# Performance work log

Hardware: AMD Instinct MI355X
Metric: run time of the kernel (lower is better)

Reference implementation:

```python
import jax, jax.numpy as jnp
import numpy as np

LAMADA = 0.0001
USER_NUM, ITEM_NUM, FACTOR = 100000, 50000, 64
N_EDGES, BATCH = 3200000, 4096


def setup_inputs() -> dict:
    key = jax.random.key(0)
    ks = jax.random.split(key, 11)
    return {
        "embed_user": jax.random.normal(ks[0], (USER_NUM, FACTOR), jnp.float32) * 0.01,
        "embed_item": jax.random.normal(ks[1], (ITEM_NUM, FACTOR), jnp.float32) * 0.01,
        "u_idx": jax.random.randint(ks[2], (N_EDGES,), 0, USER_NUM, jnp.int32),
        "i_idx": jax.random.randint(ks[3], (N_EDGES,), 0, ITEM_NUM, jnp.int32),
        "ui_vals": jax.random.uniform(ks[4], (N_EDGES,), jnp.float32),
        "iu_vals": jax.random.uniform(ks[5], (N_EDGES,), jnp.float32),
        "d_i": jax.random.uniform(ks[6], (USER_NUM,), jnp.float32),
        "d_j": jax.random.uniform(ks[7], (ITEM_NUM,), jnp.float32),
        "user": jax.random.randint(ks[8], (BATCH,), 0, USER_NUM, jnp.int32),
        "item_i": jax.random.randint(ks[9], (BATCH,), 0, ITEM_NUM, jnp.int32),
        "item_j": jax.random.randint(ks[10], (BATCH,), 0, ITEM_NUM, jnp.int32),
    }


def _spmm_u(i_emb, u_idx, i_idx, vals):
    # user_item_matrix @ items_embedding  (COO SpMM via segment_sum)
    msg = i_emb[i_idx] * vals[:, None]  # [E, F]
    return jax.ops.segment_sum(msg, u_idx, num_segments=USER_NUM)


def _spmm_i(u_emb, u_idx, i_idx, vals):
    # item_user_matrix @ users_embedding
    msg = u_emb[u_idx] * vals[:, None]  # [E, F]
    return jax.ops.segment_sum(msg, i_idx, num_segments=ITEM_NUM)


def reference(embed_user, embed_item, u_idx, i_idx, ui_vals, iu_vals,
              d_i, d_j, user, item_i, item_j):
    di = d_i[:, None]  # [U,1] broadcast == expand(-1, factor_num)
    dj = d_j[:, None]  # [I,1]

    gcn1_u = _spmm_u(embed_item, u_idx, i_idx, ui_vals) + embed_user * di
    gcn1_i = _spmm_i(embed_user, u_idx, i_idx, iu_vals) + embed_item * dj
    gcn2_u = _spmm_u(gcn1_i, u_idx, i_idx, ui_vals) + gcn1_u * di
    gcn2_i = _spmm_i(gcn1_u, u_idx, i_idx, iu_vals) + gcn1_i * dj

    gcn_u = embed_user + gcn1_u + gcn2_u
    gcn_i = embed_item + gcn1_i + gcn2_i

    u = gcn_u[user]        # [B, F]
    pi = gcn_i[item_i]     # [B, F]
    pj = gcn_i[item_j]     # [B, F]

    pred_i = jnp.sum(u * pi, axis=-1)
    pred_j = jnp.sum(u * pj, axis=-1)

    l2 = LAMADA * jnp.mean(u ** 2) + LAMADA * jnp.mean(pi ** 2 + pj ** 2)
    # -log(sigmoid(x)) == softplus(-x), numerically stable
    loss2 = jnp.mean(jax.nn.softplus(-(pred_i - pred_j)))
    return loss2 + l2
```

## Files before the change

### kernel.cpp

```cpp
#include <hip/hip_runtime.h>
#include <math.h>

#define USER_NUM 100000
#define ITEM_NUM 50000
#define FACTOR   64
#define LAMADA   0.0001f

#define RB_BITS 7
#define RB      128
#define NBU   782
#define NBI   391
#define CAPU  5120
#define CAPI  9216
#define CHUNK 8192

#define FP8_SCALE    256.0f
#define FP8_INVSCALE 0.00390625f

typedef unsigned short ushort_t;
typedef unsigned int   uint_t;
typedef float v2f_t __attribute__((ext_vector_type(2)));

__device__ __forceinline__ void dec8(uint2 t, float* __restrict__ f) {
    v2f_t p0 = __builtin_amdgcn_cvt_pk_f32_fp8(t.x, false);
    v2f_t p1 = __builtin_amdgcn_cvt_pk_f32_fp8(t.x, true);
    v2f_t p2 = __builtin_amdgcn_cvt_pk_f32_fp8(t.y, false);
    v2f_t p3 = __builtin_amdgcn_cvt_pk_f32_fp8(t.y, true);
    f[0] = p0.x; f[1] = p0.y; f[2] = p1.x; f[3] = p1.y;
    f[4] = p2.x; f[5] = p2.y; f[6] = p3.x; f[7] = p3.y;
}
__device__ __forceinline__ uint_t enc1(float v) {
    return (uint_t)__builtin_amdgcn_cvt_pk_fp8_f32(v, v, 0, false) & 0xFFu;
}
__device__ __forceinline__ float decv(uint_t e) {
    v2f_t p = __builtin_amdgcn_cvt_pk_f32_fp8(e, false);
    return p.x;
}

__device__ __forceinline__ void acc8p(uint2 t, float v, v2f_t* __restrict__ S) {
    v2f_t vv = {v, v};
    S[0] = __builtin_elementwise_fma(vv, __builtin_amdgcn_cvt_pk_f32_fp8(t.x, false), S[0]);
    S[1] = __builtin_elementwise_fma(vv, __builtin_amdgcn_cvt_pk_f32_fp8(t.x, true),  S[1]);
    S[2] = __builtin_elementwise_fma(vv, __builtin_amdgcn_cvt_pk_f32_fp8(t.y, false), S[2]);
    S[3] = __builtin_elementwise_fma(vv, __builtin_amdgcn_cvt_pk_f32_fp8(t.y, true),  S[3]);
}

__global__ void to_fp8_both(const float* __restrict__ a, int n4a,
                            const float* __restrict__ b, int n4b,
                            unsigned char* __restrict__ da, unsigned char* __restrict__ db) {
    int gid = blockIdx.x * blockDim.x + threadIdx.x;
    const float* src; unsigned char* dst; int idx;
    if (gid < n4a) { src = a; dst = da; idx = gid; }
    else if (gid < n4a + n4b) { src = b; dst = db; idx = gid - n4a; }
    else return;
    float4 v = ((const float4*)src)[idx];
    int r = __builtin_amdgcn_cvt_pk_fp8_f32(v.x * FP8_SCALE, v.y * FP8_SCALE, 0, false);
    r = __builtin_amdgcn_cvt_pk_fp8_f32(v.z * FP8_SCALE, v.w * FP8_SCALE, r, true);
    ((uint_t*)dst)[idx] = (uint_t)r;
}

__global__ void init_cursors(int* __restrict__ cur_u, int* __restrict__ cur_i) {
    int t = blockIdx.x * blockDim.x + threadIdx.x;
    if (t < NBU) cur_u[t] = t * CAPU;
    if (t < NBI) cur_i[t] = t * CAPI;
}

__device__ __forceinline__ void place_phase(
    const int* __restrict__ rows_idx, const int* __restrict__ cols_idx,
    const float* __restrict__ vals, int* __restrict__ cur,
    uint_t* __restrict__ staged, int nb, int start, int end,
    uint_t* __restrict__ s_stage, int* __restrict__ s_cnt,
    int* __restrict__ s_scan, int* __restrict__ s_gbase) {
    int tid = threadIdx.x;
    int len = end - start;
    s_cnt[tid] = 0;
    __syncthreads();
    int vend = start + (len & ~3);
    for (int e = start + tid * 4; e < vend; e += 4096) {
        int4 r = *(const int4*)(rows_idx + e);
        atomicAdd(&s_cnt[r.x >> RB_BITS], 1);
        atomicAdd(&s_cnt[r.y >> RB_BITS], 1);
        atomicAdd(&s_cnt[r.z >> RB_BITS], 1);
        atomicAdd(&s_cnt[r.w >> RB_BITS], 1);
    }
    for (int e = vend + tid; e < end; e += 1024) {
        atomicAdd(&s_cnt[rows_idx[e] >> RB_BITS], 1);
    }
    __syncthreads();
    int c = s_cnt[tid];
    s_scan[tid] = c;
    __syncthreads();
    #pragma unroll
    for (int off = 1; off < 1024; off <<= 1) {
        int v = (tid >= off) ? s_scan[tid - off] : 0;
        __syncthreads();
        s_scan[tid] += v;
        __syncthreads();
    }
    int excl = s_scan[tid] - c;
    __syncthreads();
    s_scan[tid] = excl;
    if (tid < nb) {
        s_gbase[tid] = c ? atomicAdd(&cur[tid], c) : 0;
        s_cnt[tid] = excl;
    }
    __syncthreads();
    for (int e = start + tid * 4; e < vend; e += 4096) {
        int4 r = *(const int4*)(rows_idx + e);
        int4 cc = *(const int4*)(cols_idx + e);
        float4 v = *(const float4*)(vals + e);
        int p0 = atomicAdd(&s_cnt[r.x >> RB_BITS], 1);
        int p1 = atomicAdd(&s_cnt[r.y >> RB_BITS], 1);
        int p2 = atomicAdd(&s_cnt[r.z >> RB_BITS], 1);
        int p3 = atomicAdd(&s_cnt[r.w >> RB_BITS], 1);
        s_stage[p0] = ((uint_t)(r.x & (RB-1)) << 25) | ((uint_t)cc.x << 8) | enc1(v.x);
        s_stage[p1] = ((uint_t)(r.y & (RB-1)) << 25) | ((uint_t)cc.y << 8) | enc1(v.y);
        s_stage[p2] = ((uint_t)(r.z & (RB-1)) << 25) | ((uint_t)cc.z << 8) | enc1(v.z);
        s_stage[p3] = ((uint_t)(r.w & (RB-1)) << 25) | ((uint_t)cc.w << 8) | enc1(v.w);
    }
    for (int e = vend + tid; e < end; e += 1024) {
        int rr = rows_idx[e];
        int p = atomicAdd(&s_cnt[rr >> RB_BITS], 1);
        s_stage[p] = ((uint_t)(rr & (RB-1)) << 25) | ((uint_t)cols_idx[e] << 8) | enc1(vals[e]);
    }
    __syncthreads();
    for (int t = tid; t < len; t += 1024) {
        int lo = 0, hi = nb;
        while (hi - lo > 1) {
            int mid = (lo + hi) >> 1;
            if (s_scan[mid] <= t) lo = mid; else hi = mid;
        }
        staged[s_gbase[lo] + (t - s_scan[lo])] = s_stage[t];
    }
    __syncthreads();
}

__global__ __launch_bounds__(1024) void place2(
        const int* __restrict__ u_idx, const int* __restrict__ i_idx,
        const float* __restrict__ ui_vals, const float* __restrict__ iu_vals,
        int* __restrict__ cur_u, int* __restrict__ cur_i,
        uint_t* __restrict__ staged_u, uint_t* __restrict__ staged_i, int n_edges) {
    __shared__ uint_t s_stage[CHUNK];
    __shared__ int s_cnt[1024];
    __shared__ int s_scan[1025];
    __shared__ int s_gbase[1024];
    int start = blockIdx.x * CHUNK;
    int end = min(start + CHUNK, n_edges);
    if (start >= end) return;
    place_phase(u_idx, i_idx, ui_vals, cur_u, staged_u, NBU, start, end,
                s_stage, s_cnt, s_scan, s_gbase);
    place_phase(i_idx, u_idx, iu_vals, cur_i, staged_i, NBI, start, end,
                s_stage, s_cnt, s_scan, s_gbase);
}

__global__ void bucket_finalize(const uint_t* __restrict__ staged, const int* __restrict__ cur,
                                int cap, int* __restrict__ ptr, uint_t* __restrict__ cs,
                                int n_rows) {
    __shared__ int s_cnt[RB];
    __shared__ int s_pos[RB];
    int b = blockIdx.x, tid = threadIdx.x;
    int sbase = b * cap;
    int nE = cur[b] - sbase;
    if (tid < RB) s_cnt[tid] = 0;
    __syncthreads();
    int nE8 = nE & ~7;
    for (int k = tid * 8; k < nE8; k += 2048) {
        uint4 a = *(const uint4*)(staged + sbase + k);
        uint4 c = *(const uint4*)(staged + sbase + k + 4);
        atomicAdd(&s_cnt[a.x >> 25], 1); atomicAdd(&s_cnt[a.y >> 25], 1);
        atomicAdd(&s_cnt[a.z >> 25], 1); atomicAdd(&s_cnt[a.w >> 25], 1);
        atomicAdd(&s_cnt[c.x >> 25], 1); atomicAdd(&s_cnt[c.y >> 25], 1);
        atomicAdd(&s_cnt[c.z >> 25], 1); atomicAdd(&s_cnt[c.w >> 25], 1);
    }
    if (tid == 0) for (int k = nE8; k < nE; ++k) atomicAdd(&s_cnt[staged[sbase + k] >> 25], 1);
    __syncthreads();
    int x = (tid < RB) ? s_cnt[tid] : 0;
    if (tid < RB) s_pos[tid] = x;
    __syncthreads();
    for (int off = 1; off < RB; off <<= 1) {
        int t = (tid < RB && tid >= off) ? s_pos[tid - off] : 0;
        __syncthreads();
        if (tid < RB) s_pos[tid] += t;
        __syncthreads();
    }
    if (tid < RB) {
        int excl = s_pos[tid] - x + sbase;
        int r = (b << RB_BITS) + tid;
        if (r < n_rows) ptr[r + b] = excl;
        s_pos[tid] = excl;
    }
    if (tid == 0) ptr[min((b << RB_BITS) + RB, n_rows) + b] = sbase + nE;
    __syncthreads();
    for (int k = tid * 8; k < nE8; k += 2048) {
        uint4 a = *(const uint4*)(staged + sbase + k);
        uint4 c = *(const uint4*)(staged + sbase + k + 4);
        int p0 = atomicAdd(&s_pos[a.x >> 25], 1);
        int p1 = atomicAdd(&s_pos[a.y >> 25], 1);
        int p2 = atomicAdd(&s_pos[a.z >> 25], 1);
        int p3 = atomicAdd(&s_pos[a.w >> 25], 1);
        int p4 = atomicAdd(&s_pos[c.x >> 25], 1);
        int p5 = atomicAdd(&s_pos[c.y >> 25], 1);
        int p6 = atomicAdd(&s_pos[c.z >> 25], 1);
        int p7 = atomicAdd(&s_pos[c.w >> 25], 1);
        cs[p0] = a.x & 0x01FFFFFFu; cs[p1] = a.y & 0x01FFFFFFu;
        cs[p2] = a.z & 0x01FFFFFFu; cs[p3] = a.w & 0x01FFFFFFu;
        cs[p4] = c.x & 0x01FFFFFFu; cs[p5] = c.y & 0x01FFFFFFu;
        cs[p6] = c.z & 0x01FFFFFFu; cs[p7] = c.w & 0x01FFFFFFu;
    }
    if (tid == 0) for (int k = nE8; k < nE; ++k) {
        uint_t se = staged[sbase + k];
        int pos = atomicAdd(&s_pos[se >> 25], 1);
        cs[pos] = se & 0x01FFFFFFu;
    }
}

__device__ __forceinline__ void gather_dot8f8(const uint_t* __restrict__ cs, int start, int end,
                                              const uint2* __restrict__ tab2, int g, int l,
                                              float* __restrict__ acc) {
    v2f_t A[4] = {{0.f,0.f},{0.f,0.f},{0.f,0.f},{0.f,0.f}};
    v2f_t B[4] = {{0.f,0.f},{0.f,0.f},{0.f,0.f},{0.f,0.f}};
    const uint2* __restrict__ tl = tab2 + l;
    int k = start;
    for (; k + 32 <= end; k += 32) {
        uint_t c0 = cs[k + g];
        uint_t c1 = cs[k + 8 + g];
        uint_t c2 = cs[k + 16 + g];
        uint_t c3 = cs[k + 24 + g];
        uint2 t0 = tl[(c0 >> 8) << 3];
        uint2 t1 = tl[(c1 >> 8) << 3];
        uint2 t2 = tl[(c2 >> 8) << 3];
        uint2 t3 = tl[(c3 >> 8) << 3];
        float v0 = decv(c0);
        float v1 = decv(c1);
        float v2 = decv(c2);
        float v3 = decv(c3);
        acc8p(t0, v0, A);
        acc8p(t1, v1, B);
        acc8p(t2, v2, A);
        acc8p(t3, v3, B);
    }
    if (k + 16 <= end) {
        uint_t c0 = cs[k + g];
        uint_t c1 = cs[k + 8 + g];
        uint2 t0 = tl[(c0 >> 8) << 3];
        uint2 t1 = tl[(c1 >> 8) << 3];
        acc8p(t0, decv(c0), A);
        acc8p(t1, decv(c1), B);
        k += 16;
    }
    if (k + 8 <= end) {
        uint_t c0 = cs[k + g];
        uint2 t0 = tl[(c0 >> 8) << 3];
        acc8p(t0, decv(c0), A);
        k += 8;
    }
    if (k + g < end) {
        uint_t c0 = cs[k + g];
        uint2 t0 = tl[(c0 >> 8) << 3];
        acc8p(t0, decv(c0), B);
    }
    #pragma unroll
    for (int i = 0; i < 4; ++i) {
        v2f_t s = A[i] + B[i];
        float r0 = s.x, r1 = s.y;
        r0 += __shfl_xor(r0, 8, 64);
        r1 += __shfl_xor(r1, 8, 64);
        r0 += __shfl_xor(r0, 16, 64);
        r1 += __shfl_xor(r1, 16, 64);
        r0 += __shfl_xor(r0, 32, 64);
        r1 += __shfl_xor(r1, 32, 64);
        acc[2 * i]     = r0;
        acc[2 * i + 1] = r1;
    }
}

__global__ void csr_spmm5(const int* __restrict__ ptr_u, const uint_t* __restrict__ cs_u,
                          const int* __restrict__ ptr_i, const uint_t* __restrict__ cs_i,
                          const uint2* __restrict__ beu2, const uint2* __restrict__ bei2,
                          const float* __restrict__ eu, const float* __restrict__ ei,
                          const float* __restrict__ d_i, const float* __restrict__ d_j,
                          uint2* __restrict__ g1u2, uint2* __restrict__ g1i2) {
    int w = (blockIdx.x * blockDim.x + threadIdx.x) >> 6;
    int lane = threadIdx.x & 63;
    int g = lane >> 3, l = lane & 7;
    const int* ptr; const uint_t* cs; const uint2* src; const float* self;
    const float* d; uint2* out; int row;
    if (w < USER_NUM) {
        row = w; ptr = ptr_u; cs = cs_u; src = bei2; self = eu; d = d_i; out = g1u2;
    } else if (w < USER_NUM + ITEM_NUM) {
        row = w - USER_NUM; ptr = ptr_i; cs = cs_i; src = beu2; self = ei; d = d_j; out = g1i2;
    } else return;
    int pidx = row + (row >> RB_BITS);
    int start = ptr[pidx], end = ptr[pidx + 1];
    float acc[8];
    gather_dot8f8(cs, start, end, src, g, l, acc);
    if (g == 0) {
        float4 s0 = ((const float4*)self)[(size_t)row * 16 + l * 2];
        float4 s1 = ((const float4*)self)[(size_t)row * 16 + l * 2 + 1];
        float dv = d[row] * FP8_SCALE;
        float o0 = acc[0] + s0.x * dv, o1 = acc[1] + s0.y * dv;
        float o2 = acc[2] + s0.z * dv, o3 = acc[3] + s0.w * dv;
        float o4 = acc[4] + s1.x * dv, o5 = acc[5] + s1.y * dv;
        float o6 = acc[6] + s1.z * dv, o7 = acc[7] + s1.w * dv;
        int r0 = __builtin_amdgcn_cvt_pk_fp8_f32(o0, o1, 0, false);
        r0 = __builtin_amdgcn_cvt_pk_fp8_f32(o2, o3, r0, true);
        int r1 = __builtin_amdgcn_cvt_pk_fp8_f32(o4, o5, 0, false);
        r1 = __builtin_amdgcn_cvt_pk_fp8_f32(o6, o7, r1, true);
        uint2 o; o.x = (uint_t)r0; o.y = (uint_t)r1;
        out[(size_t)row * 8 + l] = o;
    }
}

__global__ void gather_rows(const float* __restrict__ eu, const float* __restrict__ ei,
                            const uint2* __restrict__ g1u2, const uint2* __restrict__ g1i2,
                            const int* __restrict__ ptr_u, const uint_t* __restrict__ cs_u,
                            const int* __restrict__ ptr_i, const uint_t* __restrict__ cs_i,
                            const float* __restrict__ d_i, const float* __restrict__ d_j,
                            const int* __restrict__ user, const int* __restrict__ item_i,
                            const int* __restrict__ item_j, float* __restrict__ rows, int batch) {
    int w = (blockIdx.x * blockDim.x + threadIdx.x) >> 6;
    int lane = threadIdx.x & 63;
    int g = lane >> 3, l = lane & 7;
    if (w >= 3 * batch) return;
    int role = w / batch;
    int s = w - role * batch;
    int row; const int* ptr; const uint_t* cs; const uint2* tab; const uint2* g1t;
    const float* self; float sc;
    if (role == 0) {
        row = user[s]; ptr = ptr_u; cs = cs_u; tab = g1i2; g1t = g1u2;
        self = eu; sc = 1.f + d_i[row];
    } else {
        row = (role == 1) ? item_i[s] : item_j[s];
        ptr = ptr_i; cs = cs_i; tab = g1u2; g1t = g1i2;
        self = ei; sc = 1.f + d_j[row];
    }
    int pidx = row + (row >> RB_BITS);
    float acc[8];
    gather_dot8f8(cs, ptr[pidx], ptr[pidx + 1], tab, g, l, acc);
    if (g == 0) {
        uint2 gg = g1t[(size_t)row * 8 + l];
        float gf[8];
        dec8(gg, gf);
        float4 e0 = ((const float4*)self)[(size_t)row * 16 + l * 2];
        float4 e1 = ((const float4*)self)[(size_t)row * 16 + l * 2 + 1];
        float4 o0, o1;
        o0.x = e0.x + (gf[0] * sc + acc[0]) * FP8_INVSCALE;
        o0.y = e0.y + (gf[1] * sc + acc[1]) * FP8_INVSCALE;
        o0.z = e0.z + (gf[2] * sc + acc[2]) * FP8_INVSCALE;
        o0.w = e0.w + (gf[3] * sc + acc[3]) * FP8_INVSCALE;
        o1.x = e1.x + (gf[4] * sc + acc[4]) * FP8_INVSCALE;
        o1.y = e1.y + (gf[5] * sc + acc[5]) * FP8_INVSCALE;
        o1.z = e1.z + (gf[6] * sc + acc[6]) * FP8_INVSCALE;
        o1.w = e1.w + (gf[7] * sc + acc[7]) * FP8_INVSCALE;
        ((float4*)rows)[(size_t)w * 16 + l * 2]     = o0;
        ((float4*)rows)[(size_t)w * 16 + l * 2 + 1] = o1;
    }
}

__global__ void loss_dots(const float* __restrict__ rows, float* __restrict__ partials,
                          int batch, int nblocks) {
    __shared__ float s_su2[4], s_sp2[4], s_sp[4];
    int w = (blockIdx.x * blockDim.x + threadIdx.x) >> 6;
    int lane = threadIdx.x & 63;
    int wid = (threadIdx.x >> 6);
    float su2 = 0.f, sp2 = 0.f, sp = 0.f;
    if (w < batch) {
        float U  = rows[(size_t)w * FACTOR + lane];
        float Pi = rows[(size_t)(batch + w) * FACTOR + lane];
        float Pj = rows[(size_t)(2 * batch + w) * FACTOR + lane];
        float di  = U * Pi;
        float dj  = U * Pj;
        su2 = U * U;
        sp2 = Pi * Pi + Pj * Pj;
        for (int off = 32; off; off >>= 1) {
            di  += __shfl_down(di,  off, 64);
            dj  += __shfl_down(dj,  off, 64);
            su2 += __shfl_down(su2, off, 64);
            sp2 += __shfl_down(sp2, off, 64);
        }
        if (lane == 0) {
            float x = -(di - dj);
            sp = fmaxf(x, 0.f) + log1pf(expf(-fabsf(x)));
        }
    }
    if (lane == 0) { s_su2[wid] = su2; s_sp2[wid] = sp2; s_sp[wid] = sp; }
    __syncthreads();
    if (threadIdx.x == 0) {
        int b = blockIdx.x;
        partials[b]               = s_su2[0] + s_su2[1] + s_su2[2] + s_su2[3];
        partials[nblocks + b]     = s_sp2[0] + s_sp2[1] + s_sp2[2] + s_sp2[3];
        partials[2 * nblocks + b] = s_sp[0]  + s_sp[1]  + s_sp[2]  + s_sp[3];
    }
}

__global__ void reduce_partials(const float* __restrict__ partials, int nblocks,
                                float* __restrict__ out, int batch) {
    __shared__ float s0[1024], s1[1024], s2[1024];
    int tid = threadIdx.x;
    float a = 0.f, b = 0.f, c = 0.f;
    for (int k = tid; k < nblocks; k += 1024) {
        a += partials[k];
        b += partials[nblocks + k];
        c += partials[2 * nblocks + k];
    }
    s0[tid] = a; s1[tid] = b; s2[tid] = c;
    __syncthreads();
    for (int off = 512; off; off >>= 1) {
        if (tid < off) {
            s0[tid] += s0[tid + off];
            s1[tid] += s1[tid + off];
            s2[tid] += s2[tid + off];
        }
        __syncthreads();
    }
    if (tid == 0) {
        float inv_b  = 1.0f / (float)batch;
        float inv_bf = 1.0f / (float)(batch * FACTOR);
        out[0] = s2[0] * inv_b + LAMADA * s0[0] * inv_bf + LAMADA * s1[0] * inv_bf;
    }
}

__global__ void init_scale(const float* __restrict__ src, const float* __restrict__ d,
                           float* __restrict__ dst, int n_rows) {
    int gid = blockIdx.x * blockDim.x + threadIdx.x;
    int total = n_rows * 16;
    if (gid >= total) return;
    int r = gid >> 4;
    float s = d[r];
    float4 v = ((const float4*)src)[gid];
    v.x *= s; v.y *= s; v.z *= s; v.w *= s;
    ((float4*)dst)[gid] = v;
}

__global__ void edge_spmm(const float* __restrict__ srcU, const float* __restrict__ srcI,
                          float* __restrict__ dstU, float* __restrict__ dstI,
                          const int* __restrict__ u_idx, const int* __restrict__ i_idx,
                          const float* __restrict__ ui_vals, const float* __restrict__ iu_vals,
                          int n_edges) {
    long long gid = (long long)blockIdx.x * blockDim.x + threadIdx.x;
    int e = (int)(gid >> 4);
    if (e >= n_edges) return;
    int sub = ((int)gid & 15) * 4;
    int u = u_idx[e], i = i_idx[e];
    float uv = ui_vals[e], iv = iu_vals[e];
    size_t uo = (size_t)u * FACTOR + sub;
    size_t io = (size_t)i * FACTOR + sub;
    float4 a = *(const float4*)(srcI + io);
    float4 b = *(const float4*)(srcU + uo);
    float* du = dstU + uo;
    float* di = dstI + io;
    atomicAdd(du + 0, a.x * uv); atomicAdd(du + 1, a.y * uv);
    atomicAdd(du + 2, a.z * uv); atomicAdd(du + 3, a.w * uv);
    atomicAdd(di + 0, b.x * iv); atomicAdd(di + 1, b.y * iv);
    atomicAdd(di + 2, b.z * iv); atomicAdd(di + 3, b.w * iv);
}

__global__ void batch_loss(const float* __restrict__ eu, const float* __restrict__ ei,
                           const float* __restrict__ g1u, const float* __restrict__ g1i,
                           const float* __restrict__ g2u, const float* __restrict__ g2i,
                           const int* __restrict__ user, const int* __restrict__ item_i,
                           const int* __restrict__ item_j, float* __restrict__ acc, int batch) {
    int gid = blockIdx.x * blockDim.x + threadIdx.x;
    int w = gid >> 6;
    int lane = threadIdx.x & 63;
    if (w >= batch) return;
    int uu = user[w], ii = item_i[w], jj = item_j[w];
    size_t uo = (size_t)uu * FACTOR + lane;
    size_t io = (size_t)ii * FACTOR + lane;
    size_t jo = (size_t)jj * FACTOR + lane;
    float uvv = eu[uo] + g1u[uo] + g2u[uo];
    float piv = ei[io] + g1i[io] + g2i[io];
    float pjv = ei[jo] + g1i[jo] + g2i[jo];
    float di  = uvv * piv;
    float dj  = uvv * pjv;
    float su2 = uvv * uvv;
    float sp2 = piv * piv + pjv * pjv;
    for (int off = 32; off; off >>= 1) {
        di  += __shfl_down(di,  off, 64);
        dj  += __shfl_down(dj,  off, 64);
        su2 += __shfl_down(su2, off, 64);
        sp2 += __shfl_down(sp2, off, 64);
    }
    if (lane == 0) {
        float x  = -(di - dj);
        float sp = fmaxf(x, 0.f) + log1pf(expf(-fabsf(x)));
        atomicAdd(acc + 0, su2);
        atomicAdd(acc + 1, sp2);
        atomicAdd(acc + 2, sp);
    }
}

__global__ void finalize_fb(const float* __restrict__ acc, float* __restrict__ out, int batch) {
    if (threadIdx.x == 0 && blockIdx.x == 0) {
        float inv_b  = 1.0f / (float)batch;
        float inv_bf = 1.0f / (float)(batch * FACTOR);
        out[0] = acc[2] * inv_b + LAMADA * acc[0] * inv_bf + LAMADA * acc[1] * inv_bf;
    }
}

extern "C" void kernel_launch(void* const* d_in, const int* in_sizes, int n_in,
                              void* d_out, int out_size, void* d_ws, size_t ws_size,
                              hipStream_t stream) {
    const float* eu      = (const float*)d_in[0];
    const float* ei      = (const float*)d_in[1];
    const int*   u_idx   = (const int*)d_in[2];
    const int*   i_idx   = (const int*)d_in[3];
    const float* ui_vals = (const float*)d_in[4];
    const float* iu_vals = (const float*)d_in[5];
    const float* d_i     = (const float*)d_in[6];
    const float* d_j     = (const float*)d_in[7];
    const int*   user    = (const int*)d_in[8];
    const int*   item_i  = (const int*)d_in[9];
    const int*   item_j  = (const int*)d_in[10];
    int n_edges = in_sizes[2];
    int batch   = in_sizes[8];
    float* out  = (float*)d_out;

    const size_t FU = (size_t)USER_NUM * FACTOR;
    const size_t FI = (size_t)ITEM_NUM * FACTOR;
    const size_t CU_SZ = (size_t)NBU * CAPU;
    const size_t CI_SZ = (size_t)NBI * CAPI;

    const size_t APAD_BYTES = (FU + FI) * 2;
    unsigned char* g1u8 = (unsigned char*)d_ws;
    unsigned char* g1i8 = g1u8 + FU;
    unsigned char* beu8 = g1i8 + FI;
    unsigned char* bei8 = beu8 + FU;
    uint_t* cs_u  = (uint_t*)((char*)d_ws + APAD_BYTES);
    uint_t* cs_i  = cs_u + CU_SZ;
    uint_t* staged_u = (uint_t*)d_ws;
    uint_t* staged_i = cs_u;
    int*   ptr_u = (int*)(cs_i + CI_SZ);
    int*   ptr_i = ptr_u + (USER_NUM + NBU + 2);
    int*   cur_u = ptr_i + (ITEM_NUM + NBI + 2);
    int*   cur_i = cur_u + NBU;
    float* rows  = (float*)(cur_i + NBI);
    int    nblk_loss = (batch * 64 + 255) / 256;
    float* partials = rows + (size_t)3 * batch * FACTOR;

    size_t need_bytes = ((size_t)(partials + (size_t)3 * nblk_loss) - (size_t)d_ws);

    if (ws_size >= need_bytes) {
        int nb1 = (n_edges + CHUNK - 1) / CHUNK;

        init_cursors<<<(NBU + 255) / 256, 256, 0, stream>>>(cur_u, cur_i);
        place2<<<nb1, 1024, 0, stream>>>(u_idx, i_idx, ui_vals, iu_vals,
                                         cur_u, cur_i, staged_u, staged_i, n_edges);
        bucket_finalize<<<NBI, 256, 0, stream>>>(staged_i, cur_i, CAPI, ptr_i, cs_i, ITEM_NUM);
        bucket_finalize<<<NBU, 256, 0, stream>>>(staged_u, cur_u, CAPU, ptr_u, cs_u, USER_NUM);

        int n4u = (int)(FU / 4), n4i = (int)(FI / 4);
        to_fp8_both<<<(n4u + n4i + 255) / 256, 256, 0, stream>>>(eu, n4u, ei, n4i, beu8, bei8);

        int total_waves = USER_NUM + ITEM_NUM;
        csr_spmm5<<<(total_waves * 64 + 255) / 256, 256, 0, stream>>>(
            ptr_u, cs_u, ptr_i, cs_i, (const uint2*)beu8, (const uint2*)bei8,
            eu, ei, d_i, d_j, (uint2*)g1u8, (uint2*)g1i8);

        gather_rows<<<(3 * batch * 64 + 255) / 256, 256, 0, stream>>>(
            eu, ei, (const uint2*)g1u8, (const uint2*)g1i8,
            ptr_u, cs_u, ptr_i, cs_i, d_i, d_j, user, item_i, item_j, rows, batch);
        loss_dots<<<nblk_loss, 256, 0, stream>>>(rows, partials, batch, nblk_loss);
        reduce_partials<<<1, 1024, 0, stream>>>(partials, nblk_loss, out, batch);
    } else {
        float* f_g1u = (float*)d_ws;
        float* f_g1i = f_g1u + FU;
        float* f_g2u = f_g1i + FI;
        float* f_g2i = f_g2u + FU;
        float* f_acc = f_g2i + FI;
        hipMemsetAsync(f_acc, 0, 4 * sizeof(float), stream);
        long long tot = (long long)n_edges * 16;
        int eblocks = (int)((tot + 255) / 256);
        init_scale<<<(USER_NUM * 16 + 255) / 256, 256, 0, stream>>>(eu, d_i, f_g1u, USER_NUM);
        init_scale<<<(ITEM_NUM * 16 + 255) / 256, 256, 0, stream>>>(ei, d_j, f_g1i, ITEM_NUM);
        edge_spmm<<<eblocks, 256, 0, stream>>>(eu, ei, f_g1u, f_g1i, u_idx, i_idx, ui_vals, iu_vals, n_edges);
        init_scale<<<(USER_NUM * 16 + 255) / 256, 256, 0, stream>>>(f_g1u, d_i, f_g2u, USER_NUM);
        init_scale<<<(ITEM_NUM * 16 + 255) / 256, 256, 0, stream>>>(f_g1i, d_j, f_g2i, ITEM_NUM);
        edge_spmm<<<eblocks, 256, 0, stream>>>(f_g1u, f_g1i, f_g2u, f_g2i, u_idx, i_idx, ui_vals, iu_vals, n_edges);
        batch_loss<<<(batch * 64 + 255) / 256, 256, 0, stream>>>(eu, ei, f_g1u, f_g1i, f_g2u, f_g2i,
                                                                 user, item_i, item_j, f_acc, batch);
        finalize_fb<<<1, 64, 0, stream>>>(f_acc, out, batch);
    }
}
```

Measured before the change: 311.9 us.

## Use wave-shuffle scans, bucket-tag scatter, wider finalize, two rows per wave SpMM

The placement kernel replaces its 1024-wide shared-memory Hillis-Steele scan with a wave shuffle scan plus per-wave offsets. It also records each staged edge's bucket in a ushort array, so the scatter loop no longer needs a binary search. Bucket finalize now runs 1024 threads per block, uses per-wave histograms and a shuffle scan, and keeps fewer barriers. The SpMM kernel processes two rows per wave, interleaving their gathers for more memory-level parallelism, and reduces with 64-bit packed shuffles; the cost is extra shared memory and registers and lanes idling when two rows differ in length.

New measurement: 333.7 us. 1.07x slower.

```diff
diff --git a/kernel.cpp b/kernel.cpp
--- a/kernel.cpp
+++ b/kernel.cpp
@@ -70,8 +70,10 @@
     const float* __restrict__ vals, int* __restrict__ cur,
     uint_t* __restrict__ staged, int nb, int start, int end,
     uint_t* __restrict__ s_stage, int* __restrict__ s_cnt,
-    int* __restrict__ s_scan, int* __restrict__ s_gbase) {
+    int* __restrict__ s_scan, int* __restrict__ s_gbase,
+    ushort_t* __restrict__ s_bkt, int* __restrict__ s_wsum) {
     int tid = threadIdx.x;
+    int lane = tid & 63, wid = tid >> 6;
     int len = end - start;
     s_cnt[tid] = 0;
     __syncthreads();
@@ -88,49 +90,49 @@
     }
     __syncthreads();
     int c = s_cnt[tid];
-    s_scan[tid] = c;
-    __syncthreads();
+    int v = c;
     #pragma unroll
-    for (int off = 1; off < 1024; off <<= 1) {
-        int v = (tid >= off) ? s_scan[tid - off] : 0;
-        __syncthreads();
-        s_scan[tid] += v;
-        __syncthreads();
-    }
-    int excl = s_scan[tid] - c;
-    __syncthreads();
+    for (int off = 1; off < 64; off <<= 1) {
+        int t = __shfl_up(v, off, 64);
+        if (lane >= off) v += t;
+    }
+    if (lane == 63) s_wsum[wid] = v;
+    __syncthreads();
+    int woff = 0;
+    for (int i = 0; i < wid; ++i) woff += s_wsum[i];
+    int excl = v - c + woff;
     s_scan[tid] = excl;
-    if (tid < nb) {
-        s_gbase[tid] = c ? atomicAdd(&cur[tid], c) : 0;
-        s_cnt[tid] = excl;
-    }
+    s_cnt[tid] = excl;
+    if (tid < nb) s_gbase[tid] = c ? atomicAdd(&cur[tid], c) : 0;
     __syncthreads();
     for (int e = start + tid * 4; e < vend; e += 4096) {
         int4 r = *(const int4*)(rows_idx + e);
         int4 cc = *(const int4*)(cols_idx + e);
-        float4 v = *(const float4*)(vals + e);
-        int p0 = atomicAdd(&s_cnt[r.x >> RB_BITS], 1);
-        int p1 = atomicAdd(&s_cnt[r.y >> RB_BITS], 1);
-        int p2 = atomicAdd(&s_cnt[r.z >> RB_BITS], 1);
-        int p3 = atomicAdd(&s_cnt[r.w >> RB_BITS], 1);
-        s_stage[p0] = ((uint_t)(r.x & (RB-1)) << 25) | ((uint_t)cc.x << 8) | enc1(v.x);
-        s_stage[p1] = ((uint_t)(r.y & (RB-1)) << 25) | ((uint_t)cc.y << 8) | enc1(v.y);
-        s_stage[p2] = ((uint_t)(r.z & (RB-1)) << 25) | ((uint_t)cc.z << 8) | enc1(v.z);
-        s_stage[p3] = ((uint_t)(r.w & (RB-1)) << 25) | ((uint_t)cc.w << 8) | enc1(v.w);
+        float4 v4 = *(const float4*)(vals + e);
+        int b0 = r.x >> RB_BITS, b1 = r.y >> RB_BITS;
+        int b2 = r.z >> RB_BITS, b3 = r.w >> RB_BITS;
+        int p0 = atomicAdd(&s_cnt[b0], 1);
+        int p1 = atomicAdd(&s_cnt[b1], 1);
+        int p2 = atomicAdd(&s_cnt[b2], 1);
+        int p3 = atomicAdd(&s_cnt[b3], 1);
+        s_stage[p0] = ((uint_t)(r.x & (RB-1)) << 25) | ((uint_t)cc.x << 8) | enc1(v4.x);
+        s_stage[p1] = ((uint_t)(r.y & (RB-1)) << 25) | ((uint_t)cc.y << 8) | enc1(v4.y);
+        s_stage[p2] = ((uint_t)(r.z & (RB-1)) << 25) | ((uint_t)cc.z << 8) | enc1(v4.z);
+        s_stage[p3] = ((uint_t)(r.w & (RB-1)) << 25) | ((uint_t)cc.w << 8) | enc1(v4.w);
+        s_bkt[p0] = (ushort_t)b0; s_bkt[p1] = (ushort_t)b1;
+        s_bkt[p2] = (ushort_t)b2; s_bkt[p3] = (ushort_t)b3;
     }
     for (int e = vend + tid; e < end; e += 1024) {
         int rr = rows_idx[e];
-        int p = atomicAdd(&s_cnt[rr >> RB_BITS], 1);
+        int b0 = rr >> RB_BITS;
+        int p = atomicAdd(&s_cnt[b0], 1);
         s_stage[p] = ((uint_t)(rr & (RB-1)) << 25) | ((uint_t)cols_idx[e] << 8) | enc1(vals[e]);
+        s_bkt[p] = (ushort_t)b0;
     }
     __syncthreads();
     for (int t = tid; t < len; t += 1024) {
-        int lo = 0, hi = nb;
-        while (hi - lo > 1) {
-            int mid = (lo + hi) >> 1;
-            if (s_scan[mid] <= t) lo = mid; else hi = mid;
-        }
-        staged[s_gbase[lo] + (t - s_scan[lo])] = s_stage[t];
+        int b = s_bkt[t];
+        staged[s_gbase[b] + (t - s_scan[b])] = s_stage[t];
     }
     __syncthreads();
 }
@@ -142,70 +144,79 @@
         uint_t* __restrict__ staged_u, uint_t* __restrict__ staged_i, int n_edges) {
     __shared__ uint_t s_stage[CHUNK];
     __shared__ int s_cnt[1024];
-    __shared__ int s_scan[1025];
+    __shared__ int s_scan[1024];
     __shared__ int s_gbase[1024];
+    __shared__ ushort_t s_bkt[CHUNK];
+    __shared__ int s_wsum[16];
     int start = blockIdx.x * CHUNK;
     int end = min(start + CHUNK, n_edges);
     if (start >= end) return;
     place_phase(u_idx, i_idx, ui_vals, cur_u, staged_u, NBU, start, end,
-                s_stage, s_cnt, s_scan, s_gbase);
+                s_stage, s_cnt, s_scan, s_gbase, s_bkt, s_wsum);
     place_phase(i_idx, u_idx, iu_vals, cur_i, staged_i, NBI, start, end,
-                s_stage, s_cnt, s_scan, s_gbase);
-}
-
-__global__ void bucket_finalize(const uint_t* __restrict__ staged, const int* __restrict__ cur,
-                                int cap, int* __restrict__ ptr, uint_t* __restrict__ cs,
-                                int n_rows) {
-    __shared__ int s_cnt[RB];
+                s_stage, s_cnt, s_scan, s_gbase, s_bkt, s_wsum);
+}
+
+__global__ __launch_bounds__(1024) void bucket_finalize2(
+        const uint_t* __restrict__ staged, const int* __restrict__ cur,
+        int cap, int* __restrict__ ptr, uint_t* __restrict__ cs, int n_rows) {
+    __shared__ int s_hist[16][RB];
     __shared__ int s_pos[RB];
+    __shared__ int s_w[2];
     int b = blockIdx.x, tid = threadIdx.x;
+    int lane = tid & 63, wid = tid >> 6;
     int sbase = b * cap;
     int nE = cur[b] - sbase;
-    if (tid < RB) s_cnt[tid] = 0;
+    for (int i = tid; i < 16 * RB; i += 1024) ((int*)s_hist)[i] = 0;
     __syncthreads();
     int nE8 = nE & ~7;
-    for (int k = tid * 8; k < nE8; k += 2048) {
+    for (int k = tid * 8; k < nE8; k += 8192) {
         uint4 a = *(const uint4*)(staged + sbase + k);
-        uint4 c = *(const uint4*)(staged + sbase + k + 4);
-        atomicAdd(&s_cnt[a.x >> 25], 1); atomicAdd(&s_cnt[a.y >> 25], 1);
-        atomicAdd(&s_cnt[a.z >> 25], 1); atomicAdd(&s_cnt[a.w >> 25], 1);
-        atomicAdd(&s_cnt[c.x >> 25], 1); atomicAdd(&s_cnt[c.y >> 25], 1);
-        atomicAdd(&s_cnt[c.z >> 25], 1); atomicAdd(&s_cnt[c.w >> 25], 1);
-    }
-    if (tid == 0) for (int k = nE8; k < nE; ++k) atomicAdd(&s_cnt[staged[sbase + k] >> 25], 1);
-    __syncthreads();
-    int x = (tid < RB) ? s_cnt[tid] : 0;
-    if (tid < RB) s_pos[tid] = x;
-    __syncthreads();
-    for (int off = 1; off < RB; off <<= 1) {
-        int t = (tid < RB && tid >= off) ? s_pos[tid - off] : 0;
-        __syncthreads();
-        if (tid < RB) s_pos[tid] += t;
-        __syncthreads();
-    }
+        uint4 c4 = *(const uint4*)(staged + sbase + k + 4);
+        atomicAdd(&s_hist[wid][a.x >> 25], 1);  atomicAdd(&s_hist[wid][a.y >> 25], 1);
+        atomicAdd(&s_hist[wid][a.z >> 25], 1);  atomicAdd(&s_hist[wid][a.w >> 25], 1);
+        atomicAdd(&s_hist[wid][c4.x >> 25], 1); atomicAdd(&s_hist[wid][c4.y >> 25], 1);
+        atomicAdd(&s_hist[wid][c4.z >> 25], 1); atomicAdd(&s_hist[wid][c4.w >> 25], 1);
+    }
+    if (tid == 0) for (int k = nE8; k < nE; ++k) atomicAdd(&s_hist[0][staged[sbase + k] >> 25], 1);
+    __syncthreads();
+    int c = 0, v = 0;
     if (tid < RB) {
-        int excl = s_pos[tid] - x + sbase;
+        #pragma unroll
+        for (int w2 = 0; w2 < 16; ++w2) c += s_hist[w2][tid];
+        v = c;
+        #pragma unroll
+        for (int off = 1; off < 64; off <<= 1) {
+            int t = __shfl_up(v, off, 64);
+            if (lane >= off) v += t;
+        }
+        if (lane == 63) s_w[wid] = v;
+    }
+    __syncthreads();
+    if (tid < RB) {
+        if (wid == 1) v += s_w[0];
+        int excl = v - c + sbase;
         int r = (b << RB_BITS) + tid;
         if (r < n_rows) ptr[r + b] = excl;
         s_pos[tid] = excl;
     }
     if (tid == 0) ptr[min((b << RB_BITS) + RB, n_rows) + b] = sbase + nE;
     __syncthreads();
-    for (int k = tid * 8; k < nE8; k += 2048) {
+    for (int k = tid * 8; k < nE8; k += 8192) {
         uint4 a = *(const uint4*)(staged + sbase + k);
-        uint4 c = *(const uint4*)(staged + sbase + k + 4);
+        uint4 c4 = *(const uint4*)(staged + sbase + k + 4);
         int p0 = atomicAdd(&s_pos[a.x >> 25], 1);
         int p1 = atomicAdd(&s_pos[a.y >> 25], 1);
         int p2 = atomicAdd(&s_pos[a.z >> 25], 1);
         int p3 = atomicAdd(&s_pos[a.w >> 25], 1);
-        int p4 = atomicAdd(&s_pos[c.x >> 25], 1);
-        int p5 = atomicAdd(&s_pos[c.y >> 25], 1);
-        int p6 = atomicAdd(&s_pos[c.z >> 25], 1);
-        int p7 = atomicAdd(&s_pos[c.w >> 25], 1);
-        cs[p0] = a.x & 0x01FFFFFFu; cs[p1] = a.y & 0x01FFFFFFu;
-        cs[p2] = a.z & 0x01FFFFFFu; cs[p3] = a.w & 0x01FFFFFFu;
-        cs[p4] = c.x & 0x01FFFFFFu; cs[p5] = c.y & 0x01FFFFFFu;
-        cs[p6] = c.z & 0x01FFFFFFu; cs[p7] = c.w & 0x01FFFFFFu;
+        int p4 = atomicAdd(&s_pos[c4.x >> 25], 1);
+        int p5 = atomicAdd(&s_pos[c4.y >> 25], 1);
+        int p6 = atomicAdd(&s_pos[c4.z >> 25], 1);
+        int p7 = atomicAdd(&s_pos[c4.w >> 25], 1);
+        cs[p0] = a.x & 0x01FFFFFFu;  cs[p1] = a.y & 0x01FFFFFFu;
+        cs[p2] = a.z & 0x01FFFFFFu;  cs[p3] = a.w & 0x01FFFFFFu;
+        cs[p4] = c4.x & 0x01FFFFFFu; cs[p5] = c4.y & 0x01FFFFFFu;
+        cs[p6] = c4.z & 0x01FFFFFFu; cs[p7] = c4.w & 0x01FFFFFFu;
     }
     if (tid == 0) for (int k = nE8; k < nE; ++k) {
         uint_t se = staged[sbase + k];
@@ -214,31 +225,27 @@
     }
 }
 
-__device__ __forceinline__ void gather_dot8f8(const uint_t* __restrict__ cs, int start, int end,
-                                              const uint2* __restrict__ tab2, int g, int l,
-                                              float* __restrict__ acc) {
-    v2f_t A[4] = {{0.f,0.f},{0.f,0.f},{0.f,0.f},{0.f,0.f}};
-    v2f_t B[4] = {{0.f,0.f},{0.f,0.f},{0.f,0.f},{0.f,0.f}};
-    const uint2* __restrict__ tl = tab2 + l;
-    int k = start;
-    for (; k + 32 <= end; k += 32) {
-        uint_t c0 = cs[k + g];
-        uint_t c1 = cs[k + 8 + g];
-        uint_t c2 = cs[k + 16 + g];
-        uint_t c3 = cs[k + 24 + g];
-        uint2 t0 = tl[(c0 >> 8) << 3];
-        uint2 t1 = tl[(c1 >> 8) << 3];
-        uint2 t2 = tl[(c2 >> 8) << 3];
-        uint2 t3 = tl[(c3 >> 8) << 3];
-        float v0 = decv(c0);
-        float v1 = decv(c1);
-        float v2 = decv(c2);
-        float v3 = decv(c3);
-        acc8p(t0, v0, A);
-        acc8p(t1, v1, B);
-        acc8p(t2, v2, A);
-        acc8p(t3, v3, B);
-    }
+__device__ __forceinline__ void gd_step32(const uint_t* __restrict__ cs, int k, int g,
+                                          const uint2* __restrict__ tl,
+                                          v2f_t* __restrict__ A, v2f_t* __restrict__ B) {
+    uint_t c0 = cs[k + g];
+    uint_t c1 = cs[k + 8 + g];
+    uint_t c2 = cs[k + 16 + g];
+    uint_t c3 = cs[k + 24 + g];
+    uint2 t0 = tl[(c0 >> 8) << 3];
+    uint2 t1 = tl[(c1 >> 8) << 3];
+    uint2 t2 = tl[(c2 >> 8) << 3];
+    uint2 t3 = tl[(c3 >> 8) << 3];
+    acc8p(t0, decv(c0), A);
+    acc8p(t1, decv(c1), B);
+    acc8p(t2, decv(c2), A);
+    acc8p(t3, decv(c3), B);
+}
+
+__device__ __forceinline__ void gd_rest(const uint_t* __restrict__ cs, int k, int end, int g,
+                                        const uint2* __restrict__ tl,
+                                        v2f_t* __restrict__ A, v2f_t* __restrict__ B) {
+    for (; k + 32 <= end; k += 32) gd_step32(cs, k, g, tl, A, B);
     if (k + 16 <= end) {
         uint_t c0 = cs[k + g];
         uint_t c1 = cs[k + 8 + g];
@@ -259,22 +266,36 @@
         uint2 t0 = tl[(c0 >> 8) << 3];
         acc8p(t0, decv(c0), B);
     }
+}
+
+__device__ __forceinline__ void reduce_pk(v2f_t* __restrict__ A, v2f_t* __restrict__ B,
+                                          float* __restrict__ acc) {
     #pragma unroll
     for (int i = 0; i < 4; ++i) {
         v2f_t s = A[i] + B[i];
-        float r0 = s.x, r1 = s.y;
-        r0 += __shfl_xor(r0, 8, 64);
-        r1 += __shfl_xor(r1, 8, 64);
-        r0 += __shfl_xor(r0, 16, 64);
-        r1 += __shfl_xor(r1, 16, 64);
-        r0 += __shfl_xor(r0, 32, 64);
-        r1 += __shfl_xor(r1, 32, 64);
-        acc[2 * i]     = r0;
-        acc[2 * i + 1] = r1;
-    }
-}
-
-__global__ void csr_spmm5(const int* __restrict__ ptr_u, const uint_t* __restrict__ cs_u,
+        #pragma unroll
+        for (int m = 8; m <= 32; m <<= 1) {
+            union { double d; v2f_t v; } u;
+            u.v = s;
+            u.d = __shfl_xor(u.d, m, 64);
+            s += u.v;
+        }
+        acc[2 * i]     = s.x;
+        acc[2 * i + 1] = s.y;
+    }
+}
+
+__device__ __forceinline__ void gather_dot8f8(const uint_t* __restrict__ cs, int start, int end,
+                                              const uint2* __restrict__ tab2, int g, int l,
+                                              float* __restrict__ acc) {
+    v2f_t A[4] = {{0.f,0.f},{0.f,0.f},{0.f,0.f},{0.f,0.f}};
+    v2f_t B[4] = {{0.f,0.f},{0.f,0.f},{0.f,0.f},{0.f,0.f}};
+    const uint2* __restrict__ tl = tab2 + l;
+    gd_rest(cs, start, end, g, tl, A, B);
+    reduce_pk(A, B, acc);
+}
+
+__global__ void csr_spmm6(const int* __restrict__ ptr_u, const uint_t* __restrict__ cs_u,
                           const int* __restrict__ ptr_i, const uint_t* __restrict__ cs_i,
                           const uint2* __restrict__ beu2, const uint2* __restrict__ bei2,
                           const float* __restrict__ eu, const float* __restrict__ ei,
@@ -283,25 +304,45 @@
     int w = (blockIdx.x * blockDim.x + threadIdx.x) >> 6;
     int lane = threadIdx.x & 63;
     int g = lane >> 3, l = lane & 7;
+    int rp = w << 1;
     const int* ptr; const uint_t* cs; const uint2* src; const float* self;
-    const float* d; uint2* out; int row;
-    if (w < USER_NUM) {
-        row = w; ptr = ptr_u; cs = cs_u; src = bei2; self = eu; d = d_i; out = g1u2;
-    } else if (w < USER_NUM + ITEM_NUM) {
-        row = w - USER_NUM; ptr = ptr_i; cs = cs_i; src = beu2; self = ei; d = d_j; out = g1i2;
+    const float* d; uint2* out; int row0;
+    if (rp < USER_NUM) {
+        row0 = rp; ptr = ptr_u; cs = cs_u; src = bei2; self = eu; d = d_i; out = g1u2;
+    } else if (rp < USER_NUM + ITEM_NUM) {
+        row0 = rp - USER_NUM; ptr = ptr_i; cs = cs_i; src = beu2; self = ei; d = d_j; out = g1i2;
     } else return;
-    int pidx = row + (row >> RB_BITS);
-    int start = ptr[pidx], end = ptr[pidx + 1];
-    float acc[8];
-    gather_dot8f8(cs, start, end, src, g, l, acc);
-    if (g == 0) {
+    int row1 = row0 + 1;
+    int pi0 = row0 + (row0 >> RB_BITS);
+    int pi1 = row1 + (row1 >> RB_BITS);
+    int k0 = ptr[pi0], e0 = ptr[pi0 + 1];
+    int k1 = ptr[pi1], e1 = ptr[pi1 + 1];
+    const uint2* __restrict__ tl = src + l;
+    v2f_t A0[4] = {{0.f,0.f},{0.f,0.f},{0.f,0.f},{0.f,0.f}};
+    v2f_t B0[4] = {{0.f,0.f},{0.f,0.f},{0.f,0.f},{0.f,0.f}};
+    v2f_t A1[4] = {{0.f,0.f},{0.f,0.f},{0.f,0.f},{0.f,0.f}};
+    v2f_t B1[4] = {{0.f,0.f},{0.f,0.f},{0.f,0.f},{0.f,0.f}};
+    for (; k0 + 32 <= e0 && k1 + 32 <= e1; k0 += 32, k1 += 32) {
+        gd_step32(cs, k0, g, tl, A0, B0);
+        gd_step32(cs, k1, g, tl, A1, B1);
+    }
+    gd_rest(cs, k0, e0, g, tl, A0, B0);
+    gd_rest(cs, k1, e1, g, tl, A1, B1);
+    float acc0[8], acc1[8];
+    reduce_pk(A0, B0, acc0);
+    reduce_pk(A1, B1, acc1);
+    if (g < 2) {
+        int row = g ? row1 : row0;
+        float av[8];
+        #pragma unroll
+        for (int i = 0; i < 8; ++i) av[i] = g ? acc1[i] : acc0[i];
         float4 s0 = ((const float4*)self)[(size_t)row * 16 + l * 2];
         float4 s1 = ((const float4*)self)[(size_t)row * 16 + l * 2 + 1];
         float dv = d[row] * FP8_SCALE;
-        float o0 = acc[0] + s0.x * dv, o1 = acc[1] + s0.y * dv;
-        float o2 = acc[2] + s0.z * dv, o3 = acc[3] + s0.w * dv;
-        float o4 = acc[4] + s1.x * dv, o5 = acc[5] + s1.y * dv;
-        float o6 = acc[6] + s1.z * dv, o7 = acc[7] + s1.w * dv;
+        float o0 = av[0] + s0.x * dv, o1 = av[1] + s0.y * dv;
+        float o2 = av[2] + s0.z * dv, o3 = av[3] + s0.w * dv;
+        float o4 = av[4] + s1.x * dv, o5 = av[5] + s1.y * dv;
+        float o6 = av[6] + s1.z * dv, o7 = av[7] + s1.w * dv;
         int r0 = __builtin_amdgcn_cvt_pk_fp8_f32(o0, o1, 0, false);
         r0 = __builtin_amdgcn_cvt_pk_fp8_f32(o2, o3, r0, true);
         int r1 = __builtin_amdgcn_cvt_pk_fp8_f32(o4, o5, 0, false);
@@ -546,14 +587,14 @@
         init_cursors<<<(NBU + 255) / 256, 256, 0, stream>>>(cur_u, cur_i);
         place2<<<nb1, 1024, 0, stream>>>(u_idx, i_idx, ui_vals, iu_vals,
                                          cur_u, cur_i, staged_u, staged_i, n_edges);
-        bucket_finalize<<<NBI, 256, 0, stream>>>(staged_i, cur_i, CAPI, ptr_i, cs_i, ITEM_NUM);
-        bucket_finalize<<<NBU, 256, 0, stream>>>(staged_u, cur_u, CAPU, ptr_u, cs_u, USER_NUM);
+        bucket_finalize2<<<NBI, 1024, 0, stream>>>(staged_i, cur_i, CAPI, ptr_i, cs_i, ITEM_NUM);
+        bucket_finalize2<<<NBU, 1024, 0, stream>>>(staged_u, cur_u, CAPU, ptr_u, cs_u, USER_NUM);
 
         int n4u = (int)(FU / 4), n4i = (int)(FI / 4);
         to_fp8_both<<<(n4u + n4i + 255) / 256, 256, 0, stream>>>(eu, n4u, ei, n4i, beu8, bei8);
 
-        int total_waves = USER_NUM + ITEM_NUM;
-        csr_spmm5<<<(total_waves * 64 + 255) / 256, 256, 0, stream>>>(
+        int nwave2 = (USER_NUM + ITEM_NUM) / 2;
+        csr_spmm6<<<(nwave2 * 64 + 255) / 256, 256, 0, stream>>>(
             ptr_u, cs_u, ptr_i, cs_i, (const uint2*)beu8, (const uint2*)bei8,
             eu, ei, d_i, d_j, (uint2*)g1u8, (uint2*)g1i8);
 
```
